# Optimization experiments

Measured on AMD Instinct MI355X. Metric: run time of the kernel, lower is better.

Reference implementation:

```python
import jax, jax.numpy as jnp
import numpy as np

N, E, B = 80000, 480000, 800  # nodes, edges, graphs
H, C = 4, 64                  # attention heads, per-head channels

def gelu(x):
    return jax.nn.gelu(x, approximate=False)

def setup_inputs() -> dict:
    key = jax.random.key(0)
    ks = jax.random.split(key, 40)
    nrm = lambda k, shp, s=0.1: jax.random.normal(k, shp, jnp.float32) * s
    inp = {
        'x': jax.random.normal(ks[0], (N, 21), jnp.float32),
        'edge_index': jax.random.randint(ks[1], (2, E), 0, N, dtype=jnp.int32),
        'batch_idx': jnp.sort(jax.random.randint(ks[2], (N,), 0, B, dtype=jnp.int32)),
        'rnafm': jax.random.normal(ks[3], (B, 640), jnp.float32),
        'hand_feat': jax.random.normal(ks[4], (B, 40), jnp.float32),
        # GATConv params: lin weight [H*C, in], att_src/att_dst [H, C], bias [C]
        'g1_W': nrm(ks[5], (H * C, 21)), 'g1_as': nrm(ks[6], (H, C)), 'g1_ad': nrm(ks[7], (H, C)), 'g1_b': nrm(ks[8], (C,)),
        'g2_W': nrm(ks[9], (H * C, C)), 'g2_as': nrm(ks[10], (H, C)), 'g2_ad': nrm(ks[11], (H, C)), 'g2_b': nrm(ks[12], (C,)),
        'g3_W': nrm(ks[13], (H * C, C)), 'g3_as': nrm(ks[14], (H, C)), 'g3_ad': nrm(ks[15], (H, C)), 'g3_b': nrm(ks[16], (C,)),
        'pool_W': nrm(ks[17], (1, C)), 'pool_b': nrm(ks[18], (1,)),
        'e1_W': nrm(ks[19], (256, 744)), 'e1_b': nrm(ks[20], (256,)),
        'ln_g': jnp.ones((256,), jnp.float32), 'ln_b': jnp.zeros((256,), jnp.float32),
        'e2_W': nrm(ks[21], (128, 256)), 'e2_b': nrm(ks[22], (128,)),
        'bin_W': nrm(ks[23], (1, 128)), 'bin_b': nrm(ks[24], (1,)),
        'ad1_W': nrm(ks[25], (5, 32, 128)), 'ad1_b': nrm(ks[26], (5, 32)),
        'ad2_W': nrm(ks[27], (5, 1, 32)), 'ad2_b': nrm(ks[28], (5, 1)),
        'c1_W': nrm(ks[29], (64, 128)), 'c1_b': nrm(ks[30], (64,)),
        'c2_W': nrm(ks[31], (6, 64)), 'c2_b': nrm(ks[32], (6,)),
    }
    return inp


def reference(x, edge_index, batch_idx, rnafm, hand_feat,
              g1_W, g1_as, g1_ad, g1_b,
              g2_W, g2_as, g2_ad, g2_b,
              g3_W, g3_as, g3_ad, g3_b,
              pool_W, pool_b, e1_W, e1_b, ln_g, ln_b, e2_W, e2_b,
              bin_W, bin_b, ad1_W, ad1_b, ad2_W, ad2_b, c1_W, c1_b, c2_W, c2_b):
    n = x.shape[0]
    # PyG GATConv default: add self loops
    loops = jnp.arange(n, dtype=edge_index.dtype)
    ei = jnp.concatenate([edge_index, jnp.stack([loops, loops])], axis=1)
    src, dst = ei[0], ei[1]

    def gat(h_in, W, a_s, a_d, b):
        h = (h_in @ W.T).reshape(n, H, C)              # [N,H,C]
        s = (h * a_s[None]).sum(-1)                    # [N,H] att_src . h
        d = (h * a_d[None]).sum(-1)                    # [N,H]
        e = jax.nn.leaky_relu(s[src] + d[dst], 0.2)    # [E',H]
        m = jax.ops.segment_max(e, dst, num_segments=n)
        ex = jnp.exp(e - m[dst])                       # segment softmax (stable)
        z = jax.ops.segment_sum(ex, dst, num_segments=n)
        alpha = ex / z[dst]                            # [E',H]
        out = jax.ops.segment_sum(h[src] * alpha[:, :, None], dst, num_segments=n)
        return out.mean(axis=1) + b                    # concat=False -> mean heads

    h = gelu(gat(x, g1_W, g1_as, g1_ad, g1_b))
    h = gelu(gat(h, g2_W, g2_as, g2_ad, g2_b))
    h = gelu(gat(h, g3_W, g3_as, g3_ad, g3_b))

    # attention-weighted pooling; softmax over ALL nodes (dim=0), as in source
    attn = jax.nn.softmax(h @ pool_W.T + pool_b, axis=0)   # [N,1]
    pooled = jax.ops.segment_sum(h * attn, batch_idx, num_segments=B)  # [B,64]

    fused = jnp.concatenate([pooled, rnafm, hand_feat], axis=-1)       # [B,744]
    z1 = gelu(fused @ e1_W.T + e1_b)
    mu = z1.mean(-1, keepdims=True)
    var = ((z1 - mu) ** 2).mean(-1, keepdims=True)
    z1 = (z1 - mu) / jnp.sqrt(var + 1e-5) * ln_g + ln_b
    shared = gelu(z1 @ e2_W.T + e2_b)                      # [B,128]

    binary = (shared @ bin_W.T + bin_b)[:, 0]              # [B]
    h1 = gelu(jnp.einsum('bd,ehd->ebh', shared, ad1_W) + ad1_b[:, None, :])
    per = jnp.einsum('ebh,eh->eb', h1, ad2_W[:, 0, :]) + ad2_b  # [5,B]
    cls = gelu(shared @ c1_W.T + c1_b) @ c2_W.T + c2_b     # [B,6]
    return binary, per, cls
```

## Files before the change

### kernel.cpp

```cpp
#include <hip/hip_runtime.h>
#include <hip/hip_bf16.h>
#include <math.h>

constexpr int N_NODES = 80000;
constexpr int N_EDGES = 480000;
constexpr int N_B     = 800;
constexpr int PADDEG  = 64;

typedef __attribute__((ext_vector_type(8))) short bf16x8;
typedef __attribute__((ext_vector_type(4))) float f32x4;

__device__ __forceinline__ float gelu_exact(float x) {
    return 0.5f * x * (1.0f + erff(x * 0.70710678118654752f));
}
__device__ __forceinline__ float lrelu(float v) {
    return v > 0.f ? v : 0.2f * v;
}
__device__ __forceinline__ unsigned short f2bf(float f) {
    unsigned u = __float_as_uint(f);
    unsigned r = u + 0x7FFFu + ((u >> 16) & 1u);
    return (unsigned short)(r >> 16);
}
__device__ __forceinline__ float bf2f(unsigned short h) {
    return __uint_as_float(((unsigned)h) << 16);
}

template<int IN_DIM>
__launch_bounds__(256, 2)
__global__ void gat_transform(const float* __restrict__ xin,
                              const float* __restrict__ W,
                              const float* __restrict__ aS,
                              const float* __restrict__ aD,
                              unsigned short* __restrict__ hfull,
                              float* __restrict__ sArr,
                              float* __restrict__ dArr) {
    constexpr int K  = (IN_DIM + 31) & ~31;
    constexpr int KS = K / 32;
    constexpr int KP = K + 8;
    __shared__ __align__(16) unsigned short Wb[256 * KP];
    __shared__ __align__(16) unsigned short xs[32 * KP];

    const int tid = threadIdx.x;
    const int lane = tid & 63, w = tid >> 6;

    for (int idx = tid; idx < 256 * K; idx += 256) {
        int c = idx / K, k = idx - c * K;
        Wb[c * KP + k] = (k < IN_DIM) ? f2bf(W[c * IN_DIM + k]) : (unsigned short)0;
    }
    __syncthreads();

    bf16x8 bfrag[4][KS];
    float asv[4], adv[4];
#pragma unroll
    for (int t = 0; t < 4; ++t) {
        const int ch = w * 64 + t * 16 + (lane & 15);
#pragma unroll
        for (int s = 0; s < KS; ++s)
            bfrag[t][s] = *reinterpret_cast<const bf16x8*>(&Wb[ch * KP + s * 32 + (lane >> 4) * 8]);
        asv[t] = aS[ch];
        adv[t] = aD[ch];
    }

    const int ntiles = N_NODES / 32;
    for (int tile = blockIdx.x; tile < ntiles; tile += gridDim.x) {
        const int n0 = tile * 32;
        __syncthreads();
        for (int idx = tid; idx < 32 * K; idx += 256) {
            int r = idx / K, k = idx - r * K;
            xs[r * KP + k] = (k < IN_DIM) ? f2bf(xin[(size_t)(n0 + r) * IN_DIM + k])
                                          : (unsigned short)0;
        }
        __syncthreads();

        f32x4 acc[2][4];
#pragma unroll
        for (int m = 0; m < 2; ++m) {
            bf16x8 afrag[KS];
#pragma unroll
            for (int s = 0; s < KS; ++s)
                afrag[s] = *reinterpret_cast<const bf16x8*>(
                    &xs[(m * 16 + (lane & 15)) * KP + s * 32 + (lane >> 4) * 8]);
#pragma unroll
            for (int t = 0; t < 4; ++t) {
                f32x4 a = {0.f, 0.f, 0.f, 0.f};
#pragma unroll
                for (int s = 0; s < KS; ++s)
                    a = __builtin_amdgcn_mfma_f32_16x16x32_bf16(afrag[s], bfrag[t][s], a, 0, 0, 0);
                acc[m][t] = a;
            }
        }

#pragma unroll
        for (int m = 0; m < 2; ++m) {
            float sv[4] = {0, 0, 0, 0}, dv[4] = {0, 0, 0, 0};
#pragma unroll
            for (int t = 0; t < 4; ++t) {
                const int ch = w * 64 + t * 16 + (lane & 15);
#pragma unroll
                for (int j = 0; j < 4; ++j) {
                    float hv = acc[m][t][j];
                    int node = n0 + m * 16 + (lane >> 4) * 4 + j;
                    hfull[(size_t)node * 256 + ch] = f2bf(hv);
                    sv[j] += hv * asv[t];
                    dv[j] += hv * adv[t];
                }
            }
#pragma unroll
            for (int j = 0; j < 4; ++j) {
                sv[j] += __shfl_xor(sv[j], 1, 64); dv[j] += __shfl_xor(dv[j], 1, 64);
                sv[j] += __shfl_xor(sv[j], 2, 64); dv[j] += __shfl_xor(dv[j], 2, 64);
                sv[j] += __shfl_xor(sv[j], 4, 64); dv[j] += __shfl_xor(dv[j], 4, 64);
                sv[j] += __shfl_xor(sv[j], 8, 64); dv[j] += __shfl_xor(dv[j], 8, 64);
                if ((lane & 15) == 0) {
                    int node = n0 + m * 16 + (lane >> 4) * 4 + j;
                    sArr[node * 4 + w] = sv[j];
                    dArr[node * 4 + w] = dv[j];
                }
            }
        }
    }
}

__global__ void csr_scatter_pad(const int* __restrict__ ei,
                                int* __restrict__ cnt, int* __restrict__ csrc) {
    int e = blockIdx.x * 256 + threadIdx.x;
    if (e >= N_EDGES) return;
    int src = ei[e], dst = ei[N_EDGES + e];
    int slot = atomicAdd(&cnt[dst], 1);
    csrc[(size_t)dst * PADDEG + slot] = src;
}

template<bool POOL>
__launch_bounds__(256)
__global__ void gat_gather(const int* __restrict__ cnt, const int* __restrict__ csrc,
                           const float* __restrict__ sArr, const float* __restrict__ dArr,
                           const unsigned short* __restrict__ hfull,
                           const float* __restrict__ bias,
                           const float* __restrict__ poolW, const float* __restrict__ poolB,
                           float* __restrict__ xout,
                           float* __restrict__ logit, float* __restrict__ pmax) {
    constexpr int CAP = PADDEG;
    __shared__ float qbuf[4][4][CAP * 4];
    __shared__ int   sbuf[4][4][CAP];
    __shared__ float red[16];

    const int wid = threadIdx.x >> 6;
    const int lane = threadIdx.x & 63;
    const int nl = lane >> 4;
    const int sub = lane & 15;
    const int n = blockIdx.x * 16 + wid * 4 + nl;

    const int jb = n * PADDEG;
    const int deg = cnt[n];

    const int hh = sub & 3;
    const int slot = sub >> 2;
    const float dv = dArr[n * 4 + hh];
    const float qself = expf(lrelu(sArr[n * 4 + hh] + dv));
    float zp = 0.f;

    for (int base = 0; base < deg; base += 4) {
        int s = base + slot;
        if (s < deg) {
            int src = csrc[jb + s];
            float q = expf(lrelu(sArr[src * 4 + hh] + dv));
            qbuf[wid][nl][s * 4 + hh] = q;
            if (hh == 0) sbuf[wid][nl][s] = src;
            zp += q;
        }
    }
    zp += __shfl_xor(zp, 4, 64);
    zp += __shfl_xor(zp, 8, 64);
    const float inv = 0.25f / (zp + qself);
    __threadfence_block();

    const int h = sub >> 2;
    const int c16 = sub * 16;
    const int bl = (lane & 48) + h;
    const float inv_g = __shfl(inv, bl, 64);
    const float qs_g  = __shfl(qself, bl, 64);

#define LOADU4(S, C) (*reinterpret_cast<const uint4*>(&hfull[(size_t)(unsigned)(S) * 256 + (C)]))
#define UNPK8(A, B, Q, U) { \
    A[B + 0] = fmaf((Q), __uint_as_float((U).x << 16),          A[B + 0]); \
    A[B + 1] = fmaf((Q), __uint_as_float((U).x & 0xFFFF0000u),  A[B + 1]); \
    A[B + 2] = fmaf((Q), __uint_as_float((U).y << 16),          A[B + 2]); \
    A[B + 3] = fmaf((Q), __uint_as_float((U).y & 0xFFFF0000u),  A[B + 3]); \
    A[B + 4] = fmaf((Q), __uint_as_float((U).z << 16),          A[B + 4]); \
    A[B + 5] = fmaf((Q), __uint_as_float((U).z & 0xFFFF0000u),  A[B + 5]); \
    A[B + 6] = fmaf((Q), __uint_as_float((U).w << 16),          A[B + 6]); \
    A[B + 7] = fmaf((Q), __uint_as_float((U).w & 0xFFFF0000u),  A[B + 7]); }

    float acc[16] = {0, 0, 0, 0, 0, 0, 0, 0, 0, 0, 0, 0, 0, 0, 0, 0};
    {
        uint4 ua = LOADU4(n, c16);
        uint4 ub = LOADU4(n, c16 + 8);
        UNPK8(acc, 0, qs_g, ua);
        UNPK8(acc, 8, qs_g, ub);
    }
    int s = 0;
    for (; s + 1 < deg; s += 2) {
        int s0 = sbuf[wid][nl][s], s1 = sbuf[wid][nl][s + 1];
        float q0 = qbuf[wid][nl][s * 4 + h];
        float q1 = qbuf[wid][nl][(s + 1) * 4 + h];
        uint4 u0a = LOADU4(s0, c16);
        uint4 u0b = LOADU4(s0, c16 + 8);
        uint4 u1a = LOADU4(s1, c16);
        uint4 u1b = LOADU4(s1, c16 + 8);
        UNPK8(acc, 0, q0, u0a);
        UNPK8(acc, 8, q0, u0b);
        UNPK8(acc, 0, q1, u1a);
        UNPK8(acc, 8, q1, u1b);
    }
    if (s < deg) {
        int s0 = sbuf[wid][nl][s];
        float q0 = qbuf[wid][nl][s * 4 + h];
        uint4 u0a = LOADU4(s0, c16);
        uint4 u0b = LOADU4(s0, c16 + 8);
        UNPK8(acc, 0, q0, u0a);
        UNPK8(acc, 8, q0, u0b);
    }
#undef UNPK8
#undef LOADU4

#pragma unroll
    for (int j = 0; j < 16; ++j) acc[j] *= inv_g;
#pragma unroll
    for (int j = 0; j < 16; ++j) {
        acc[j] += __shfl_xor(acc[j], 4, 64);
        acc[j] += __shfl_xor(acc[j], 8, 64);
    }

    const int qq = sub & 3;
    const int cc = qq * 16 + h * 4;
    float v0 = (h == 0) ? acc[0] : (h == 1) ? acc[4] : (h == 2) ? acc[8]  : acc[12];
    float v1 = (h == 0) ? acc[1] : (h == 1) ? acc[5] : (h == 2) ? acc[9]  : acc[13];
    float v2 = (h == 0) ? acc[2] : (h == 1) ? acc[6] : (h == 2) ? acc[10] : acc[14];
    float v3 = (h == 0) ? acc[3] : (h == 1) ? acc[7] : (h == 2) ? acc[11] : acc[15];
    const float4 b4 = *reinterpret_cast<const float4*>(&bias[cc]);
    float4 o4;
    o4.x = gelu_exact(v0 + b4.x);
    o4.y = gelu_exact(v1 + b4.y);
    o4.z = gelu_exact(v2 + b4.z);
    o4.w = gelu_exact(v3 + b4.w);
    *reinterpret_cast<float4*>(&xout[(size_t)n * 64 + cc]) = o4;

    if (POOL) {
        const float4 pw = *reinterpret_cast<const float4*>(&poolW[cc]);
        float p = o4.x * pw.x + o4.y * pw.y + o4.z * pw.z + o4.w * pw.w;
#pragma unroll
        for (int of = 1; of < 16; of <<= 1) p += __shfl_xor(p, of, 64);
        float lg = p + poolB[0];
        if (sub == 0) {
            logit[n] = lg;
            red[wid * 4 + nl] = lg;
        }
        __syncthreads();
        if (threadIdx.x == 0) {
            float mm = red[0];
#pragma unroll
            for (int i = 1; i < 16; ++i) mm = fmaxf(mm, red[i]);
            pmax[blockIdx.x] = mm;
        }
    }
}

__global__ void reduce_max(const float* __restrict__ pmax, int n,
                           float* __restrict__ gmax) {
    __shared__ float red[256];
    float m = -INFINITY;
    for (int i = threadIdx.x; i < n; i += 256) m = fmaxf(m, pmax[i]);
    red[threadIdx.x] = m;
    __syncthreads();
    for (int s = 128; s > 0; s >>= 1) {
        if (threadIdx.x < s) red[threadIdx.x] = fmaxf(red[threadIdx.x], red[threadIdx.x + s]);
        __syncthreads();
    }
    if (threadIdx.x == 0) *gmax = red[0];
}

__global__ void seg_bounds(const int* __restrict__ batch, int* __restrict__ start) {
    int n = blockIdx.x * 256 + threadIdx.x;
    if (n >= N_NODES) return;
    int b1 = batch[n];
    int b0 = (n == 0) ? -1 : batch[n - 1];
    for (int b = b0 + 1; b <= b1; ++b) start[b] = n;
    if (n == N_NODES - 1)
        for (int b = b1 + 1; b <= N_B; ++b) start[b] = N_NODES;
}

__global__ void pool_graph(const float* __restrict__ h3,
                           const float* __restrict__ logit,
                           const float* __restrict__ gmax,
                           const int* __restrict__ start,
                           float* __restrict__ pooled,
                           float* __restrict__ gsum) {
    __shared__ float sacc[4][64];
    __shared__ float sw[4];
    int b = blockIdx.x;
    int s = start[b], e = start[b + 1];
    int lane = threadIdx.x & 63, wid = threadIdx.x >> 6;
    float M = *gmax;
    float acc = 0.f, wsum = 0.f;
    for (int n = s + wid; n < e; n += 4) {
        float w = expf(logit[n] - M);
        acc += h3[(size_t)n * 64 + lane] * w;
        if (lane == 0) wsum += w;
    }
    sacc[wid][lane] = acc;
    if (lane == 0) sw[wid] = wsum;
    __syncthreads();
    if (wid == 0) {
        pooled[(size_t)b * 64 + lane] = sacc[0][lane] + sacc[1][lane] + sacc[2][lane] + sacc[3][lane];
        if (lane == 0) atomicAdd(gsum, sw[0] + sw[1] + sw[2] + sw[3]);
    }
}

constexpr int GB1  = 8;
constexpr int KSEG = 372;

__launch_bounds__(256, 4)
__global__ void head1_part(const float* __restrict__ pooled, const float* __restrict__ gsum,
                           const float* __restrict__ rnafm, const float* __restrict__ hand,
                           const float* __restrict__ e1W,
                           float* __restrict__ part) {
    __shared__ __align__(16) float fused[GB1][KSEG + 4];
    const int bq = blockIdx.x >> 1;
    const int ks = blockIdx.x & 1;
    const int g0 = bq * GB1;
    const int k0 = ks * KSEG;
    const int tid = threadIdx.x;
    const float inv = 1.0f / *gsum;

    for (int idx = tid; idx < GB1 * KSEG; idx += 256) {
        int g = idx / KSEG, kk = idx - g * KSEG;
        int k = kk + k0;
        int b = g0 + g;
        float v;
        if (k < 64)       v = pooled[(size_t)b * 64 + k] * inv;
        else if (k < 704) v = rnafm[(size_t)b * 640 + (k - 64)];
        else              v = hand[(size_t)b * 40 + (k - 704)];
        fused[g][kk] = v;
    }
    __syncthreads();

    const float* wr = e1W + (size_t)tid * 744 + k0;
    float a0 = 0.f, a1 = 0.f, a2 = 0.f, a3 = 0.f;
    float a4 = 0.f, a5 = 0.f, a6 = 0.f, a7 = 0.f;
    for (int q = 0; q < KSEG / 4; ++q) {
        float4 w4 = *reinterpret_cast<const float4*>(wr + q * 4);
        float4 f0 = *reinterpret_cast<const float4*>(&fused[0][q * 4]);
        float4 f1 = *reinterpret_cast<const float4*>(&fused[1][q * 4]);
        float4 f2 = *reinterpret_cast<const float4*>(&fused[2][q * 4]);
        float4 f3 = *reinterpret_cast<const float4*>(&fused[3][q * 4]);
        float4 f4 = *reinterpret_cast<const float4*>(&fused[4][q * 4]);
        float4 f5 = *reinterpret_cast<const float4*>(&fused[5][q * 4]);
        float4 f6 = *reinterpret_cast<const float4*>(&fused[6][q * 4]);
        float4 f7 = *reinterpret_cast<const float4*>(&fused[7][q * 4]);
        a0 += f0.x * w4.x + f0.y * w4.y + f0.z * w4.z + f0.w * w4.w;
        a1 += f1.x * w4.x + f1.y * w4.y + f1.z * w4.z + f1.w * w4.w;
        a2 += f2.x * w4.x + f2.y * w4.y + f2.z * w4.z + f2.w * w4.w;
        a3 += f3.x * w4.x + f3.y * w4.y + f3.z * w4.z + f3.w * w4.w;
        a4 += f4.x * w4.x + f4.y * w4.y + f4.z * w4.z + f4.w * w4.w;
        a5 += f5.x * w4.x + f5.y * w4.y + f5.z * w4.z + f5.w * w4.w;
        a6 += f6.x * w4.x + f6.y * w4.y + f6.z * w4.z + f6.w * w4.w;
        a7 += f7.x * w4.x + f7.y * w4.y + f7.z * w4.z + f7.w * w4.w;
    }
    float* po = part + ((size_t)ks * N_B + g0) * 256 + tid;
    po[0 * 256] = a0; po[1 * 256] = a1; po[2 * 256] = a2; po[3 * 256] = a3;
    po[4 * 256] = a4; po[5 * 256] = a5; po[6 * 256] = a6; po[7 * 256] = a7;
}

__launch_bounds__(256, 2)
__global__ void head_fused(const float* __restrict__ part,
                           const float* __restrict__ e1b,
                           const float* __restrict__ lng, const float* __restrict__ lnb,
                           const float* __restrict__ e2W, const float* __restrict__ e2b,
                           const float* __restrict__ binW, const float* __restrict__ binB,
                           const float* __restrict__ ad1W, const float* __restrict__ ad1b,
                           const float* __restrict__ ad2W, const float* __restrict__ ad2b,
                           const float* __restrict__ c1W, const float* __restrict__ c1b,
                           const float* __restrict__ c2W, const float* __restrict__ c2b,
                           float* __restrict__ out) {
    __shared__ float zr[4][256];
    __shared__ float red1[4][4], red2[4][4];
    __shared__ float sv[4][128];
    __shared__ float t64[4][64];
    __shared__ float h1s[4][5][32];
    __shared__ float binred[4][32];
    const int b0 = blockIdx.x * 4;
    const int tid = threadIdx.x;
    const int lane = tid & 63, wid = tid >> 6;

    const float eb = e1b[tid];
    float g0 = gelu_exact(part[(size_t)(b0 + 0) * 256 + tid] + part[((size_t)N_B + b0 + 0) * 256 + tid] + eb);
    float g1 = gelu_exact(part[(size_t)(b0 + 1) * 256 + tid] + part[((size_t)N_B + b0 + 1) * 256 + tid] + eb);
    float g2 = gelu_exact(part[(size_t)(b0 + 2) * 256 + tid] + part[((size_t)N_B + b0 + 2) * 256 + tid] + eb);
    float g3 = gelu_exact(part[(size_t)(b0 + 3) * 256 + tid] + part[((size_t)N_B + b0 + 3) * 256 + tid] + eb);

    float s10 = g0, s11 = g1, s12 = g2, s13 = g3;
    float s20 = g0 * g0, s21 = g1 * g1, s22 = g2 * g2, s23 = g3 * g3;
#pragma unroll
    for (int o = 1; o < 64; o <<= 1) {
        s10 += __shfl_xor(s10, o, 64); s11 += __shfl_xor(s11, o, 64);
        s12 += __shfl_xor(s12, o, 64); s13 += __shfl_xor(s13, o, 64);
        s20 += __shfl_xor(s20, o, 64); s21 += __shfl_xor(s21, o, 64);
        s22 += __shfl_xor(s22, o, 64); s23 += __shfl_xor(s23, o, 64);
    }
    if (lane == 0) {
        red1[wid][0] = s10; red1[wid][1] = s11; red1[wid][2] = s12; red1[wid][3] = s13;
        red2[wid][0] = s20; red2[wid][1] = s21; red2[wid][2] = s22; red2[wid][3] = s23;
    }
    __syncthreads();

    const float gN = lng[tid], bN = lnb[tid];
#pragma unroll
    for (int bb = 0; bb < 4; ++bb) {
        float s1 = red1[0][bb] + red1[1][bb] + red1[2][bb] + red1[3][bb];
        float s2 = red2[0][bb] + red2[1][bb] + red2[2][bb] + red2[3][bb];
        float mu  = s1 * (1.0f / 256.0f);
        float var = s2 * (1.0f / 256.0f) - mu * mu;
        float g = (bb == 0) ? g0 : (bb == 1) ? g1 : (bb == 2) ? g2 : g3;
        zr[bb][tid] = (g - mu) * rsqrtf(var + 1e-5f) * gN + bN;
    }
    __syncthreads();

    {
        const int ch = tid & 127, gp = tid >> 7;
        const float* wr = e2W + (size_t)ch * 256;
        const float e2bb = e2b[ch];
        float a0 = e2bb, a1 = e2bb;
        for (int k = 0; k < 256; k += 4) {
            float4 w4 = *reinterpret_cast<const float4*>(wr + k);
            float4 f0 = *reinterpret_cast<const float4*>(&zr[gp * 2][k]);
            float4 f1 = *reinterpret_cast<const float4*>(&zr[gp * 2 + 1][k]);
            a0 += f0.x * w4.x + f0.y * w4.y + f0.z * w4.z + f0.w * w4.w;
            a1 += f1.x * w4.x + f1.y * w4.y + f1.z * w4.z + f1.w * w4.w;
        }
        sv[gp * 2][ch]     = gelu_exact(a0);
        sv[gp * 2 + 1][ch] = gelu_exact(a1);
    }
    __syncthreads();

    for (int idx = tid; idx < 256 + 640; idx += 256) {
        if (idx < 256) {
            int g = idx >> 6, ch = idx & 63;
            float a = c1b[ch];
            const float* wr = c1W + (size_t)ch * 128;
            for (int k = 0; k < 128; ++k) a += sv[g][k] * wr[k];
            t64[g][ch] = gelu_exact(a);
        } else {
            int j = idx - 256;
            int g = j / 160, r = j - g * 160;
            int e = r >> 5, hh = r & 31;
            float a = ad1b[e * 32 + hh];
            const float* wr = ad1W + (size_t)(e * 32 + hh) * 128;
            for (int k = 0; k < 128; ++k) a += sv[g][k] * wr[k];
            h1s[g][e][hh] = gelu_exact(a);
        }
    }
    if (tid < 128) {
        int g = tid >> 5, r = tid & 31;
        float a = 0.f;
#pragma unroll
        for (int k = 0; k < 4; ++k) a += sv[g][r * 4 + k] * binW[r * 4 + k];
        binred[g][r] = a;
    }
    __syncthreads();

    if (tid < 24) {
        int g = tid / 6, c = tid - g * 6;
        float a = c2b[c];
        const float* wr = c2W + (size_t)c * 64;
        for (int k = 0; k < 64; ++k) a += t64[g][k] * wr[k];
        out[4800 + (size_t)(b0 + g) * 6 + c] = a;
    }
    if (tid >= 32 && tid < 52) {
        int j = tid - 32;
        int g = j / 5, e = j - g * 5;
        float a = ad2b[e];
        const float* wr = ad2W + (size_t)e * 32;
        for (int k = 0; k < 32; ++k) a += h1s[g][e][k] * wr[k];
        out[800 + (size_t)e * 800 + (b0 + g)] = a;
    }
    if (tid >= 64 && tid < 68) {
        int g = tid - 64;
        float a = binB[0];
        for (int r = 0; r < 32; ++r) a += binred[g][r];
        out[b0 + g] = a;
    }
}

extern "C" void kernel_launch(void* const* d_in, const int* in_sizes, int n_in,
                              void* d_out, int out_size, void* d_ws, size_t ws_size,
                              hipStream_t stream) {
    const float* x       = (const float*)d_in[0];
    const int*   ei      = (const int*)d_in[1];
    const int*   batch   = (const int*)d_in[2];
    const float* rnafm   = (const float*)d_in[3];
    const float* hand    = (const float*)d_in[4];
    const float* gW[3]  = {(const float*)d_in[5],  (const float*)d_in[9],  (const float*)d_in[13]};
    const float* gAs[3] = {(const float*)d_in[6],  (const float*)d_in[10], (const float*)d_in[14]};
    const float* gAd[3] = {(const float*)d_in[7],  (const float*)d_in[11], (const float*)d_in[15]};
    const float* gB[3]  = {(const float*)d_in[8],  (const float*)d_in[12], (const float*)d_in[16]};
    const float* poolW = (const float*)d_in[17];
    const float* poolB = (const float*)d_in[18];
    const float* e1W = (const float*)d_in[19]; const float* e1b = (const float*)d_in[20];
    const float* lng = (const float*)d_in[21]; const float* lnb = (const float*)d_in[22];
    const float* e2W = (const float*)d_in[23]; const float* e2b = (const float*)d_in[24];
    const float* binW = (const float*)d_in[25]; const float* binB = (const float*)d_in[26];
    const float* ad1W = (const float*)d_in[27]; const float* ad1b = (const float*)d_in[28];
    const float* ad2W = (const float*)d_in[29]; const float* ad2b = (const float*)d_in[30];
    const float* c1W = (const float*)d_in[31]; const float* c1b = (const float*)d_in[32];
    const float* c2W = (const float*)d_in[33]; const float* c2b = (const float*)d_in[34];
    float* out = (float*)d_out;

    float* ws = (float*)d_ws;
    size_t off = 0;
    unsigned short* hfull = (unsigned short*)(ws + off); off += (size_t)N_NODES * 128;
    float* xcur   = ws + off; off += (size_t)N_NODES * 64;
    float* sArr   = ws + off; off += (size_t)N_NODES * 4;
    float* dArr   = ws + off; off += (size_t)N_NODES * 4;
    int*   cnt    = (int*)(ws + off); off += N_NODES;
    int*   csrc   = (int*)(ws + off); off += (size_t)N_NODES * PADDEG;
    float* logit  = ws + off; off += N_NODES;
    float* pmax   = ws + off; off += 20000;
    float* pooled = ws + off; off += (size_t)N_B * 64;
    float* part   = ws + off; off += (size_t)2 * N_B * 256;
    int*   start  = (int*)(ws + off); off += (N_B + 1);
    float* gmax   = ws + off; off += 1;
    float* gsum   = ws + off; off += 1;

    hipMemsetAsync(cnt, 0, N_NODES * sizeof(int), stream);
    csr_scatter_pad<<<(N_EDGES + 255) / 256, 256, 0, stream>>>(ei, cnt, csrc);
    seg_bounds<<<(N_NODES + 255) / 256, 256, 0, stream>>>(batch, start);

    for (int layer = 0; layer < 3; ++layer) {
        const float* xin = (layer == 0) ? x : xcur;
        if (layer == 0)
            gat_transform<21><<<512, 256, 0, stream>>>(xin, gW[0], gAs[0], gAd[0], hfull, sArr, dArr);
        else
            gat_transform<64><<<512, 256, 0, stream>>>(xin, gW[layer], gAs[layer], gAd[layer], hfull, sArr, dArr);
        if (layer < 2)
            gat_gather<false><<<N_NODES / 16, 256, 0, stream>>>(cnt, csrc, sArr, dArr, hfull,
                                                                gB[layer], nullptr, nullptr,
                                                                xcur, nullptr, nullptr);
        else
            gat_gather<true><<<N_NODES / 16, 256, 0, stream>>>(cnt, csrc, sArr, dArr, hfull,
                                                               gB[2], poolW, poolB,
                                                               xcur, logit, pmax);
    }

    reduce_max<<<1, 256, 0, stream>>>(pmax, N_NODES / 16, gmax);
    hipMemsetAsync(gsum, 0, sizeof(float), stream);
    pool_graph<<<N_B, 256, 0, stream>>>(xcur, logit, gmax, start, pooled, gsum);

    head1_part<<<(N_B / GB1) * 2, 256, 0, stream>>>(pooled, gsum, rnafm, hand, e1W, part);
    head_fused<<<N_B / 4, 256, 0, stream>>>(part, e1b, lng, lnb, e2W, e2b,
                                            binW, binB, ad1W, ad1b, ad2W, ad2b,
                                            c1W, c1b, c2W, c2b, out);
}
```

Measured before the change: 354.1 us.

## Transpose GAT projection MFMA for vectorized stores and unroll gather by four

```diff
diff --git a/kernel.cpp b/kernel.cpp
--- a/kernel.cpp
+++ b/kernel.cpp
@@ -49,16 +49,17 @@
     }
     __syncthreads();
 
-    bf16x8 bfrag[4][KS];
-    float asv[4], adv[4];
+    bf16x8 wfrag[4][KS];
+    float4 as4[4], ad4[4];
 #pragma unroll
     for (int t = 0; t < 4; ++t) {
         const int ch = w * 64 + t * 16 + (lane & 15);
 #pragma unroll
         for (int s = 0; s < KS; ++s)
-            bfrag[t][s] = *reinterpret_cast<const bf16x8*>(&Wb[ch * KP + s * 32 + (lane >> 4) * 8]);
-        asv[t] = aS[ch];
-        adv[t] = aD[ch];
+            wfrag[t][s] = *reinterpret_cast<const bf16x8*>(&Wb[ch * KP + s * 32 + (lane >> 4) * 8]);
+        const int chb = w * 64 + t * 16 + (lane >> 4) * 4;
+        as4[t] = *reinterpret_cast<const float4*>(&aS[chb]);
+        ad4[t] = *reinterpret_cast<const float4*>(&aD[chb]);
     }
 
     const int ntiles = N_NODES / 32;
@@ -72,50 +73,34 @@
         }
         __syncthreads();
 
-        f32x4 acc[2][4];
 #pragma unroll
         for (int m = 0; m < 2; ++m) {
-            bf16x8 afrag[KS];
+            bf16x8 xfrag[KS];
 #pragma unroll
             for (int s = 0; s < KS; ++s)
-                afrag[s] = *reinterpret_cast<const bf16x8*>(
+                xfrag[s] = *reinterpret_cast<const bf16x8*>(
                     &xs[(m * 16 + (lane & 15)) * KP + s * 32 + (lane >> 4) * 8]);
+
+            const int node = n0 + m * 16 + (lane & 15);
+            float sv = 0.f, dv = 0.f;
 #pragma unroll
             for (int t = 0; t < 4; ++t) {
                 f32x4 a = {0.f, 0.f, 0.f, 0.f};
 #pragma unroll
                 for (int s = 0; s < KS; ++s)
-                    a = __builtin_amdgcn_mfma_f32_16x16x32_bf16(afrag[s], bfrag[t][s], a, 0, 0, 0);
-                acc[m][t] = a;
+                    a = __builtin_amdgcn_mfma_f32_16x16x32_bf16(wfrag[t][s], xfrag[s], a, 0, 0, 0);
+                ushort4 hb;
+                hb.x = f2bf(a[0]); hb.y = f2bf(a[1]); hb.z = f2bf(a[2]); hb.w = f2bf(a[3]);
+                const int chb = w * 64 + t * 16 + (lane >> 4) * 4;
+                *reinterpret_cast<ushort4*>(&hfull[(size_t)node * 256 + chb]) = hb;
+                sv += a[0] * as4[t].x + a[1] * as4[t].y + a[2] * as4[t].z + a[3] * as4[t].w;
+                dv += a[0] * ad4[t].x + a[1] * ad4[t].y + a[2] * ad4[t].z + a[3] * ad4[t].w;
             }
-        }
-
-#pragma unroll
-        for (int m = 0; m < 2; ++m) {
-            float sv[4] = {0, 0, 0, 0}, dv[4] = {0, 0, 0, 0};
-#pragma unroll
-            for (int t = 0; t < 4; ++t) {
-                const int ch = w * 64 + t * 16 + (lane & 15);
-#pragma unroll
-                for (int j = 0; j < 4; ++j) {
-                    float hv = acc[m][t][j];
-                    int node = n0 + m * 16 + (lane >> 4) * 4 + j;
-                    hfull[(size_t)node * 256 + ch] = f2bf(hv);
-                    sv[j] += hv * asv[t];
-                    dv[j] += hv * adv[t];
-                }
-            }
-#pragma unroll
-            for (int j = 0; j < 4; ++j) {
-                sv[j] += __shfl_xor(sv[j], 1, 64); dv[j] += __shfl_xor(dv[j], 1, 64);
-                sv[j] += __shfl_xor(sv[j], 2, 64); dv[j] += __shfl_xor(dv[j], 2, 64);
-                sv[j] += __shfl_xor(sv[j], 4, 64); dv[j] += __shfl_xor(dv[j], 4, 64);
-                sv[j] += __shfl_xor(sv[j], 8, 64); dv[j] += __shfl_xor(dv[j], 8, 64);
-                if ((lane & 15) == 0) {
-                    int node = n0 + m * 16 + (lane >> 4) * 4 + j;
-                    sArr[node * 4 + w] = sv[j];
-                    dArr[node * 4 + w] = dv[j];
-                }
+            sv += __shfl_xor(sv, 16, 64); dv += __shfl_xor(dv, 16, 64);
+            sv += __shfl_xor(sv, 32, 64); dv += __shfl_xor(dv, 32, 64);
+            if (lane < 16) {
+                sArr[node * 4 + w] = sv;
+                dArr[node * 4 + w] = dv;
             }
         }
     }
@@ -140,7 +125,7 @@
                            float* __restrict__ xout,
                            float* __restrict__ logit, float* __restrict__ pmax) {
     constexpr int CAP = PADDEG;
-    __shared__ float qbuf[4][4][CAP * 4];
+    __shared__ float qbuf[4][4][4 * CAP];
     __shared__ int   sbuf[4][4][CAP];
     __shared__ float red[16];
 
@@ -164,7 +149,7 @@
         if (s < deg) {
             int src = csrc[jb + s];
             float q = expf(lrelu(sArr[src * 4 + hh] + dv));
-            qbuf[wid][nl][s * 4 + hh] = q;
+            qbuf[wid][nl][hh * CAP + s] = q;
             if (hh == 0) sbuf[wid][nl][s] = src;
             zp += q;
         }
@@ -199,10 +184,22 @@
         UNPK8(acc, 8, qs_g, ub);
     }
     int s = 0;
+    for (; s + 3 < deg; s += 4) {
+        int4  s4 = *reinterpret_cast<const int4*>(&sbuf[wid][nl][s]);
+        float4 q4 = *reinterpret_cast<const float4*>(&qbuf[wid][nl][h * CAP + s]);
+        uint4 u0a = LOADU4(s4.x, c16); uint4 u0b = LOADU4(s4.x, c16 + 8);
+        uint4 u1a = LOADU4(s4.y, c16); uint4 u1b = LOADU4(s4.y, c16 + 8);
+        uint4 u2a = LOADU4(s4.z, c16); uint4 u2b = LOADU4(s4.z, c16 + 8);
+        uint4 u3a = LOADU4(s4.w, c16); uint4 u3b = LOADU4(s4.w, c16 + 8);
+        UNPK8(acc, 0, q4.x, u0a); UNPK8(acc, 8, q4.x, u0b);
+        UNPK8(acc, 0, q4.y, u1a); UNPK8(acc, 8, q4.y, u1b);
+        UNPK8(acc, 0, q4.z, u2a); UNPK8(acc, 8, q4.z, u2b);
+        UNPK8(acc, 0, q4.w, u3a); UNPK8(acc, 8, q4.w, u3b);
+    }
     for (; s + 1 < deg; s += 2) {
         int s0 = sbuf[wid][nl][s], s1 = sbuf[wid][nl][s + 1];
-        float q0 = qbuf[wid][nl][s * 4 + h];
-        float q1 = qbuf[wid][nl][(s + 1) * 4 + h];
+        float q0 = qbuf[wid][nl][h * CAP + s];
+        float q1 = qbuf[wid][nl][h * CAP + s + 1];
         uint4 u0a = LOADU4(s0, c16);
         uint4 u0b = LOADU4(s0, c16 + 8);
         uint4 u1a = LOADU4(s1, c16);
@@ -214,7 +211,7 @@
     }
     if (s < deg) {
         int s0 = sbuf[wid][nl][s];
-        float q0 = qbuf[wid][nl][s * 4 + h];
+        float q0 = qbuf[wid][nl][h * CAP + s];
         uint4 u0a = LOADU4(s0, c16);
         uint4 u0b = LOADU4(s0, c16 + 8);
         UNPK8(acc, 0, q0, u0a);
```

Result: no change. 354.9 us (+0.2%).
